# Performance work log

Hardware: AMD Instinct MI355X
Metric: run time of the kernel (lower is better)

The kernel has to match this reference:

```python
import jax, jax.numpy as jnp
import numpy as np

L, H, D, DH, F, V, S, B, CTX = 6, 12, 768, 64, 3072, 32000, 1024, 2, 1024
EPS = 1e-5


def layernorm(x, scale, bias):
    mu = jnp.mean(x, axis=-1, keepdims=True)
    var = jnp.mean(jnp.square(x - mu), axis=-1, keepdims=True)
    return (x - mu) * jax.lax.rsqrt(var + EPS) * scale + bias


def setup_inputs() -> dict:
    key = jax.random.key(0)
    ks = jax.random.split(key, 16)
    std = 0.02
    res_std = 0.02 * (2 * L) ** (-0.5)
    inp = {
        "X": jax.random.randint(ks[0], (B, S), 0, V),
        "emb": jax.random.normal(ks[1], (V, D), jnp.float32) * std,            # tied with head weight
        "pos_emb": jax.random.normal(ks[2], (CTX, D), jnp.float32) * 0.01,
        "Wq": jax.random.normal(ks[3], (L, H, D, DH), jnp.float32) * std,
        "bq": jnp.zeros((L, H, DH), jnp.float32),
        "Wk": jax.random.normal(ks[4], (L, H, D, DH), jnp.float32) * std,
        "bk": jnp.zeros((L, H, DH), jnp.float32),
        "Wv": jax.random.normal(ks[5], (L, H, D, DH), jnp.float32) * std,
        "bv": jnp.zeros((L, H, DH), jnp.float32),
        "Wo": jax.random.normal(ks[6], (L, H * DH, D), jnp.float32) * res_std,  # ResidualScaledLinear
        "bo": jnp.zeros((L, D), jnp.float32),
        "ln1_s": jnp.ones((L, D), jnp.float32),
        "ln1_b": jnp.zeros((L, D), jnp.float32),
        "ln2_s": jnp.ones((L, D), jnp.float32),
        "ln2_b": jnp.zeros((L, D), jnp.float32),
        "W1": jax.random.normal(ks[7], (L, D, F), jnp.float32) * std,
        "b1": jnp.zeros((L, F), jnp.float32),
        "W2": jax.random.normal(ks[8], (L, F, D), jnp.float32) * res_std,       # ResidualScaledLinear
        "b2": jnp.zeros((L, D), jnp.float32),
        "lnf_s": jnp.ones((D,), jnp.float32),
        "lnf_b": jnp.zeros((D,), jnp.float32),
        "head_b": jnp.zeros((V,), jnp.float32),
    }
    return inp


def decoder_forward(X, emb, pos_emb, Wq, bq, Wk, bk, Wv, bv, Wo, bo,
                    ln1_s, ln1_b, ln2_s, ln2_b, W1, b1, W2, b2,
                    lnf_s, lnf_b, head_b):
    seq = X.shape[1]
    x = emb[X] + pos_emb[:seq]                      # [B,S,D]
    causal = jnp.tril(jnp.ones((seq, seq), bool))   # tril mask buffer
    scale = 1.0 / jnp.sqrt(jnp.float32(DH))
    for l in range(L):
        xn = layernorm(x, ln1_s[l], ln1_b[l])
        q = jnp.einsum('bsd,hdk->bhsk', xn, Wq[l]) + bq[l][None, :, None, :]
        k = jnp.einsum('bsd,hdk->bhsk', xn, Wk[l]) + bk[l][None, :, None, :]
        v = jnp.einsum('bsd,hdk->bhsk', xn, Wv[l]) + bv[l][None, :, None, :]
        scores = jnp.einsum('bhsk,bhtk->bhst', q, k) * scale
        scores = jnp.where(causal, scores, -jnp.inf)
        attn = jax.nn.softmax(scores, axis=-1)
        out = jnp.einsum('bhst,bhtk->bshk', attn, v).reshape(x.shape[0], seq, H * DH)
        x = x + out @ Wo[l] + bo[l]
        xn2 = layernorm(x, ln2_s[l], ln2_b[l])
        x = x + jax.nn.relu(xn2 @ W1[l] + b1[l]) @ W2[l] + b2[l]
    x = layernorm(x, lnf_s, lnf_b)
    return x @ emb.T + head_b                       # tied head weight


def reference(X, emb, pos_emb, Wq, bq, Wk, bk, Wv, bv, Wo, bo,
              ln1_s, ln1_b, ln2_s, ln2_b, W1, b1, W2, b2,
              lnf_s, lnf_b, head_b):
    return decoder_forward(X, emb, pos_emb, Wq, bq, Wk, bk, Wv, bv, Wo, bo,
                           ln1_s, ln1_b, ln2_s, ln2_b, W1, b1, W2, b2,
                           lnf_s, lnf_b, head_b)
```

## Files before the change

### kernel.cpp

```cpp
#include <hip/hip_runtime.h>
#include <cstdint>
#include <cstddef>

#define CL 6
#define CH 12
#define CD 768
#define CDH 64
#define CF 3072
#define CV 32000
#define CS 1024
#define CB 2
#define CM (CB*CS)
#define CQS 2304

typedef unsigned short u16;
typedef __bf16 bf16x8 __attribute__((ext_vector_type(8)));
typedef float f32x4 __attribute__((ext_vector_type(4)));

__device__ __forceinline__ float bf2f(u16 u) {
  union { unsigned int i; float f; } c; c.i = ((unsigned int)u) << 16; return c.f;
}
__device__ __forceinline__ u16 f2bf(float f) {
  union { float f; unsigned int i; } c; c.f = f;
  unsigned int lsb = (c.i >> 16) & 1u;
  c.i += 0x7fffu + lsb;
  return (u16)(c.i >> 16);
}

__device__ __forceinline__ void gload16(const u16* g, u16* l) {
  __builtin_amdgcn_global_load_lds(
      (const __attribute__((address_space(1))) void*)g,
      (__attribute__((address_space(3))) void*)l, 16, 0, 0);
}

__global__ __launch_bounds__(256) void convert_kernel(
    const float* __restrict__ src, u16* __restrict__ dst, int total)
{
  int idx = blockIdx.x * 256 + threadIdx.x;
  if (idx < total) dst[idx] = f2bf(src[idx]);
}

__global__ __launch_bounds__(256) void embed_kernel(
    const int* __restrict__ X, const float* __restrict__ emb,
    const float* __restrict__ pos, float* __restrict__ x)
{
  int idx = blockIdx.x * 256 + threadIdx.x;
  int m = idx / CD, d = idx - m * CD;
  int s = m & (CS - 1);
  x[idx] = emb[(size_t)X[m] * CD + d] + pos[s * CD + d];
}

__global__ __launch_bounds__(256) void ln_kernel(
    const float* __restrict__ x, const float* __restrict__ gs,
    const float* __restrict__ gb, u16* __restrict__ out)
{
  __shared__ float rs[4], rss[4];
  int row = blockIdx.x, tid = threadIdx.x;
  const float* xr = x + (size_t)row * CD;
  float a0 = xr[tid], a1 = xr[tid + 256], a2 = xr[tid + 512];
  float s = a0 + a1 + a2;
  float ss = a0 * a0 + a1 * a1 + a2 * a2;
#pragma unroll
  for (int sh = 32; sh > 0; sh >>= 1) {
    s  += __shfl_xor(s, sh, 64);
    ss += __shfl_xor(ss, sh, 64);
  }
  int w = tid >> 6;
  if ((tid & 63) == 0) { rs[w] = s; rss[w] = ss; }
  __syncthreads();
  s  = rs[0] + rs[1] + rs[2] + rs[3];
  ss = rss[0] + rss[1] + rss[2] + rss[3];
  float mu = s * (1.f / CD);
  float inv = rsqrtf(ss * (1.f / CD) - mu * mu + 1e-5f);
  u16* orow = out + (size_t)row * CD;
  orow[tid]       = f2bf((a0 - mu) * inv * gs[tid]       + gb[tid]);
  orow[tid + 256] = f2bf((a1 - mu) * inv * gs[tid + 256] + gb[tid + 256]);
  orow[tid + 512] = f2bf((a2 - mu) * inv * gs[tid + 512] + gb[tid + 512]);
}

__global__ __launch_bounds__(256) void trans_kernel(
    u16* __restrict__ dst, const float* __restrict__ src, int R, int C,
    int PB, long dstL)
{
  __shared__ float st[32][65];
  int r0 = blockIdx.x * 64, c0 = blockIdx.y * 32, bz = blockIdx.z;
  const float* s = src + (size_t)bz * R * C;
  u16* d = dst + (size_t)(bz / PB) * dstL + (size_t)(bz % PB) * R * C;
  int tx = threadIdx.x & 31, ty = threadIdx.x >> 5;
#pragma unroll
  for (int i = 0; i < 8; i++) {
    int r = ty + 8 * i;
    st[tx][r] = s[(size_t)(r0 + r) * C + c0 + tx];
  }
  __syncthreads();
  int j = threadIdx.x & 15, cbase = threadIdx.x >> 4;
#pragma unroll
  for (int i = 0; i < 2; i++) {
    int c = cbase + 16 * i;
    uint2 pk;
    u16* p = (u16*)&pk;
    p[0] = f2bf(st[c][4 * j + 0]);
    p[1] = f2bf(st[c][4 * j + 1]);
    p[2] = f2bf(st[c][4 * j + 2]);
    p[3] = f2bf(st[c][4 * j + 3]);
    *(uint2*)&d[(size_t)(c0 + c) * R + r0 + 4 * j] = pk;
  }
}

__global__ __launch_bounds__(256) void biaspack_kernel(
    const float* __restrict__ bq, const float* __restrict__ bk,
    const float* __restrict__ bv, float* __restrict__ dst)
{
  int idx = blockIdx.x * 256 + threadIdx.x;
  int l = idx / CQS, c = idx - l * CQS;
  float val;
  if (c < 768)       val = bq[l * 768 + c];
  else if (c < 1536) val = bk[l * 768 + c - 768];
  else               val = bv[l * 768 + c - 1536];
  dst[idx] = val;
}

template<bool RES, bool RELU, bool OUTBF>
__global__ __launch_bounds__(256) void gemm64v3_kernel(
    const u16* __restrict__ A, const u16* __restrict__ Bt,
    const float* __restrict__ bias, const float* __restrict__ res,
    void* __restrict__ outp, int M, int N, int K)
{
  __shared__ __align__(16) u16 As[64 * 32];
  __shared__ __align__(16) u16 Bs[64 * 32];
  int tid = threadIdx.x;
  int m0 = blockIdx.y * 64, n0 = blockIdx.x * 64;
  int wv = tid >> 6, ln = tid & 63;
  int quad = ln >> 4, l16 = ln & 15;
  int wm = (wv >> 1) * 32, wn = (wv & 1) * 32;
  int srow = tid >> 2, scol = (tid & 3) * 8;
  const u16* gA = A  + (size_t)(m0 + srow) * K + scol;
  const u16* gB = Bt + (size_t)(n0 + srow) * K + scol;
  u16* lA = As + wv * 512;
  u16* lB = Bs + wv * 512;

  f32x4 acc[2][2];
  acc[0][0] = f32x4{0,0,0,0}; acc[0][1] = f32x4{0,0,0,0};
  acc[1][0] = f32x4{0,0,0,0}; acc[1][1] = f32x4{0,0,0,0};

  for (int kt = 0; kt < K; kt += 32) {
    __syncthreads();
    gload16(gA + kt, lA);
    gload16(gB + kt, lB);
    __syncthreads();
    bf16x8 af[2], bfr[2];
#pragma unroll
    for (int i = 0; i < 2; i++) {
      af[i]  = *reinterpret_cast<const bf16x8*>(&As[(wm + i * 16 + l16) * 32 + quad * 8]);
      bfr[i] = *reinterpret_cast<const bf16x8*>(&Bs[(wn + i * 16 + l16) * 32 + quad * 8]);
    }
#pragma unroll
    for (int i = 0; i < 2; i++)
#pragma unroll
      for (int j = 0; j < 2; j++)
        acc[i][j] = __builtin_amdgcn_mfma_f32_16x16x32_bf16(af[i], bfr[j], acc[i][j], 0, 0, 0);
  }

#pragma unroll
  for (int i = 0; i < 2; i++) {
    int gmb = m0 + wm + i * 16 + quad * 4;
#pragma unroll
    for (int j = 0; j < 2; j++) {
      int gn = n0 + wn + j * 16 + l16;
      float bsv = bias[gn];
#pragma unroll
      for (int rr = 0; rr < 4; rr++) {
        float val = acc[i][j][rr] + bsv;
        if (RELU) val = fmaxf(val, 0.f);
        size_t o = (size_t)(gmb + rr) * N + gn;
        if (RES) val += res[o];
        if (OUTBF) ((u16*)outp)[o] = f2bf(val);
        else       ((float*)outp)[o] = val;
      }
    }
  }
}

template<bool RES, bool RELU, bool OUTBF>
__global__ __launch_bounds__(256) void gemm128_kernel(
    const u16* __restrict__ A, const u16* __restrict__ Bt,
    const float* __restrict__ bias, const float* __restrict__ res,
    void* __restrict__ outp, int M, int N, int K)
{
  __shared__ __align__(16) u16 As[128 * 32];
  __shared__ __align__(16) u16 Bs[128 * 32];
  int tid = threadIdx.x;
  int nbm = M >> 7, nbn = N >> 7, nwg = nbm * nbn;
  int orig = blockIdx.x;
  int q8 = nwg >> 3, r8 = nwg & 7;
  int xcd = orig & 7;
  int t = ((xcd < r8) ? xcd * (q8 + 1) : r8 * (q8 + 1) + (xcd - r8) * q8) + (orig >> 3);
  int bm = t % nbm, bn = t / nbm;
  int m0 = bm << 7, n0 = bn << 7;

  int wv = tid >> 6, ln = tid & 63;
  int quad = ln >> 4, l16 = ln & 15;
  int wr = wv >> 1, wc = wv & 1;

  int srow = wv * 16 + (ln >> 2);
  int scol = (ln & 3) * 8;
  const u16* ga0 = A  + (size_t)(m0 + srow) * K + scol;
  const u16* ga1 = A  + (size_t)(m0 + srow + 64) * K + scol;
  const u16* gb0 = Bt + (size_t)(n0 + srow) * K + scol;
  const u16* gb1 = Bt + (size_t)(n0 + srow + 64) * K + scol;
  u16* lA0 = As + wv * 512;
  u16* lA1 = As + 2048 + wv * 512;
  u16* lB0 = Bs + wv * 512;
  u16* lB1 = Bs + 2048 + wv * 512;

  f32x4 acc[4][4];
#pragma unroll
  for (int i = 0; i < 4; i++)
#pragma unroll
    for (int j = 0; j < 4; j++) acc[i][j] = f32x4{0.f, 0.f, 0.f, 0.f};

  for (int kt = 0; kt < K; kt += 32) {
    __syncthreads();
    gload16(ga0 + kt, lA0);
    gload16(ga1 + kt, lA1);
    gload16(gb0 + kt, lB0);
    gload16(gb1 + kt, lB1);
    __syncthreads();
    bf16x8 af[4], bf[4];
#pragma unroll
    for (int i = 0; i < 4; i++)
      af[i] = *reinterpret_cast<const bf16x8*>(&As[(wr * 64 + i * 16 + l16) * 32 + quad * 8]);
#pragma unroll
    for (int j = 0; j < 4; j++)
      bf[j] = *reinterpret_cast<const bf16x8*>(&Bs[(wc * 64 + j * 16 + l16) * 32 + quad * 8]);
#pragma unroll
    for (int i = 0; i < 4; i++)
#pragma unroll
      for (int j = 0; j < 4; j++)
        acc[i][j] = __builtin_amdgcn_mfma_f32_16x16x32_bf16(af[i], bf[j], acc[i][j], 0, 0, 0);
  }

#pragma unroll
  for (int i = 0; i < 4; i++) {
    int gm = m0 + wr * 64 + i * 16 + quad * 4;
#pragma unroll
    for (int j = 0; j < 4; j++) {
      int gn = n0 + wc * 64 + j * 16 + l16;
      float bsv = bias[gn];
#pragma unroll
      for (int rr = 0; rr < 4; rr++) {
        float val = acc[i][j][rr] + bsv;
        if (RELU) val = fmaxf(val, 0.f);
        size_t oo = (size_t)(gm + rr) * N + gn;
        if (RES) val += res[oo];
        if (OUTBF) ((u16*)outp)[oo] = f2bf(val);
        else       ((float*)outp)[oo] = val;
      }
    }
  }
}

__global__ __launch_bounds__(256) void attn_mfma_kernel(
    const u16* __restrict__ qkv, u16* __restrict__ o)
{
  __shared__ __align__(16) u16 Ks[2][64 * 64];
  __shared__ __align__(16) u16 Vt[2][64 * 64];
  __shared__ __align__(16) u16 Ps[4 * 16 * 64];

  int tid = threadIdx.x;
  int qb = (CS / 64 - 1) - blockIdx.x;
  int h = blockIdx.y, b = blockIdx.z;
  int wid = tid >> 6, lane = tid & 63, quad = lane >> 4, l16 = lane & 15;
  int q0 = qb * 64;
  size_t bh = (size_t)b * CS * CQS + h * CDH;

  const u16* kbase = qkv + bh + 768;
  const u16* vbase = qkv + bh + 1536;

  int t4 = (tid & 15) * 4, dg = (tid >> 4) * 4;

  bf16x8 aq[2];
  {
    const u16* qrow = qkv + bh + (size_t)(q0 + wid * 16 + l16) * CQS;
#pragma unroll
    for (int ks = 0; ks < 2; ks++) {
      uint4 t = *(const uint4*)(qrow + ks * 32 + quad * 8);
      aq[ks] = *reinterpret_cast<bf16x8*>(&t);
    }
  }

  f32x4 oacc[4];
  float mrow[4], lrow[4];
#pragma unroll
  for (int j = 0; j < 4; j++) oacc[j] = f32x4{0.f, 0.f, 0.f, 0.f};
#pragma unroll
  for (int r = 0; r < 4; r++) { mrow[r] = -1e30f; lrow[r] = 0.f; }

  {
#pragma unroll
    for (int it = 0; it < 2; it++) {
      int c = it * 256 + tid;
      int row = c >> 3, c8l = c & 7;
      gload16(kbase + (size_t)row * CQS + (((c8l ^ (row & 7)) * 8)),
              &Ks[0][(it * 256 + wid * 64) * 8]);
    }
    uint2 vr[4];
#pragma unroll
    for (int i = 0; i < 4; i++)
      vr[i] = *(const uint2*)(vbase + (size_t)(t4 + i) * CQS + dg);
#pragma unroll
    for (int j = 0; j < 4; j++) {
      int d = dg + j;
      uint2 pk;
      u16* p = (u16*)&pk;
      p[0] = ((const u16*)&vr[0])[j]; p[1] = ((const u16*)&vr[1])[j];
      p[2] = ((const u16*)&vr[2])[j]; p[3] = ((const u16*)&vr[3])[j];
      *(uint2*)&Vt[0][d * 64 + (((t4 >> 3) ^ (d & 7)) * 8) + (t4 & 4)] = pk;
    }
  }

  for (int t0 = 0; t0 <= q0; t0 += 64) {
    int cur = (t0 >> 6) & 1;
    __syncthreads();
    bool hasnext = (t0 + 64 <= q0);
    uint2 vr[4];
    if (hasnext) {
      const u16* vb2 = vbase + (size_t)(t0 + 64) * CQS;
#pragma unroll
      for (int i = 0; i < 4; i++)
        vr[i] = *(const uint2*)(vb2 + (size_t)(t4 + i) * CQS + dg);
      const u16* kb2 = kbase + (size_t)(t0 + 64) * CQS;
#pragma unroll
      for (int it = 0; it < 2; it++) {
        int c = it * 256 + tid;
        int row = c >> 3, c8l = c & 7;
        gload16(kb2 + (size_t)row * CQS + (((c8l ^ (row & 7)) * 8)),
                &Ks[cur ^ 1][(it * 256 + wid * 64) * 8]);
      }
    }

    f32x4 sacc[4];
#pragma unroll
    for (int j = 0; j < 4; j++) sacc[j] = f32x4{0.f, 0.f, 0.f, 0.f};
#pragma unroll
    for (int j = 0; j < 4; j++) {
      int row = j * 16 + l16;
#pragma unroll
      for (int ks = 0; ks < 2; ks++) {
        bf16x8 bk = *reinterpret_cast<const bf16x8*>(
            &Ks[cur][row * 64 + ((((ks * 4 + quad) ^ (row & 7)) * 8))]);
        sacc[j] = __builtin_amdgcn_mfma_f32_16x16x32_bf16(aq[ks], bk, sacc[j], 0, 0, 0);
      }
    }

    int qg0 = q0 + wid * 16 + quad * 4;
#pragma unroll
    for (int j = 0; j < 4; j++) {
      int tg = t0 + j * 16 + l16;
#pragma unroll
      for (int r = 0; r < 4; r++) {
        float s = sacc[j][r] * 0.125f;
        sacc[j][r] = (tg <= qg0 + r) ? s : -1e30f;
      }
    }

#pragma unroll
    for (int r = 0; r < 4; r++) {
      float m = fmaxf(fmaxf(sacc[0][r], sacc[1][r]), fmaxf(sacc[2][r], sacc[3][r]));
#pragma unroll
      for (int sh = 1; sh < 16; sh <<= 1) m = fmaxf(m, __shfl_xor(m, sh, 64));
      float mnew = fmaxf(mrow[r], m);
      float scal = __expf(mrow[r] - mnew);
      mrow[r] = mnew;
      lrow[r] *= scal;
#pragma unroll
      for (int j = 0; j < 4; j++) oacc[j][r] *= scal;
      float sum = 0.f;
#pragma unroll
      for (int j = 0; j < 4; j++) {
        float p = __expf(sacc[j][r] - mnew);
        sacc[j][r] = p;
        sum += p;
      }
#pragma unroll
      for (int sh = 1; sh < 16; sh <<= 1) sum += __shfl_xor(sum, sh, 64);
      lrow[r] += sum;
    }

    u16* Pw = Ps + wid * 1024;
#pragma unroll
    for (int j = 0; j < 4; j++) {
      int c = (l16 >> 3) + 2 * j;
#pragma unroll
      for (int r = 0; r < 4; r++) {
        int row = quad * 4 + r;
        Pw[row * 64 + (((c ^ (row & 7)) * 8) | (l16 & 7))] = f2bf(sacc[j][r]);
      }
    }

    bf16x8 ap[2];
#pragma unroll
    for (int ks = 0; ks < 2; ks++)
      ap[ks] = *reinterpret_cast<const bf16x8*>(
          &Pw[l16 * 64 + ((((ks * 4 + quad) ^ (l16 & 7)) * 8))]);
#pragma unroll
    for (int j = 0; j < 4; j++) {
      int row = j * 16 + l16;
#pragma unroll
      for (int ks = 0; ks < 2; ks++) {
        bf16x8 bv = *reinterpret_cast<const bf16x8*>(
            &Vt[cur][row * 64 + ((((ks * 4 + quad) ^ (row & 7)) * 8))]);
        oacc[j] = __builtin_amdgcn_mfma_f32_16x16x32_bf16(ap[ks], bv, oacc[j], 0, 0, 0);
      }
    }

    if (hasnext) {
#pragma unroll
      for (int j = 0; j < 4; j++) {
        int d = dg + j;
        uint2 pk;
        u16* p = (u16*)&pk;
        p[0] = ((const u16*)&vr[0])[j]; p[1] = ((const u16*)&vr[1])[j];
        p[2] = ((const u16*)&vr[2])[j]; p[3] = ((const u16*)&vr[3])[j];
        *(uint2*)&Vt[cur ^ 1][d * 64 + (((t4 >> 3) ^ (d & 7)) * 8) + (t4 & 4)] = pk;
      }
    }
  }

#pragma unroll
  for (int r = 0; r < 4; r++) {
    float inv = 1.f / lrow[r];
    int qg = q0 + wid * 16 + quad * 4 + r;
    u16* orow = o + (size_t)b * CS * CD + h * CDH + (size_t)qg * CD;
#pragma unroll
    for (int j = 0; j < 4; j++)
      orow[j * 16 + l16] = f2bf(oacc[j][r] * inv);
  }
}

extern "C" void kernel_launch(void* const* d_in, const int* in_sizes, int n_in,
                              void* d_out, int out_size, void* d_ws, size_t ws_size,
                              hipStream_t stream) {
  const int*   X      = (const int*)d_in[0];
  const float* emb    = (const float*)d_in[1];
  const float* pos    = (const float*)d_in[2];
  const float* Wq     = (const float*)d_in[3];
  const float* bq     = (const float*)d_in[4];
  const float* Wk     = (const float*)d_in[5];
  const float* bk     = (const float*)d_in[6];
  const float* Wv     = (const float*)d_in[7];
  const float* bv     = (const float*)d_in[8];
  const float* Wo     = (const float*)d_in[9];
  const float* bo     = (const float*)d_in[10];
  const float* ln1s   = (const float*)d_in[11];
  const float* ln1b   = (const float*)d_in[12];
  const float* ln2s   = (const float*)d_in[13];
  const float* ln2b   = (const float*)d_in[14];
  const float* W1     = (const float*)d_in[15];
  const float* b1     = (const float*)d_in[16];
  const float* W2     = (const float*)d_in[17];
  const float* b2     = (const float*)d_in[18];
  const float* lnfs   = (const float*)d_in[19];
  const float* lnfb   = (const float*)d_in[20];
  const float* headb  = (const float*)d_in[21];
  (void)in_sizes; (void)n_in; (void)out_size;

  char* ws = (char*)d_ws;
  size_t off = 0;
  auto alloc = [&](size_t bytes) { void* p = ws + off; off += (bytes + 255) & ~(size_t)255; return p; };

  float* x     = (float*)alloc((size_t)CM * CD * 4);
  u16*   xn    = (u16*)  alloc((size_t)CM * CD * 2);
  u16*   qkvb  = (u16*)  alloc((size_t)CM * CQS * 2);
  u16*   ao    = (u16*)  alloc((size_t)CM * CD * 2);
  u16*   hb    = (u16*)  alloc((size_t)CM * CF * 2);
  u16*   embC  = (u16*)  alloc((size_t)CV * CD * 2);
  float* biasp = (float*)alloc((size_t)CL * CQS * 4);

  const size_t WQKV = (size_t)CQS * CD;
  const size_t WOO  = (size_t)CD * CD;
  const size_t WFF  = (size_t)CD * CF;
  size_t perLayerElems = WQKV + WOO + 2 * WFF;
  bool fused = (ws_size >= off + (size_t)CL * perLayerElems * 2 + 4096);
  int LW = fused ? CL : 1;
  u16* Wqkvt = (u16*)alloc((size_t)LW * WQKV * 2);
  u16* Wot   = (u16*)alloc((size_t)LW * WOO * 2);
  u16* W1t   = (u16*)alloc((size_t)LW * WFF * 2);
  u16* W2t   = (u16*)alloc((size_t)LW * WFF * 2);

  embed_kernel<<<CM * CD / 256, 256, 0, stream>>>(X, emb, pos, x);
  convert_kernel<<<(CV * CD) / 256, 256, 0, stream>>>(emb, embC, CV * CD);
  biaspack_kernel<<<(CL * CQS) / 256, 256, 0, stream>>>(bq, bk, bv, biasp);

  if (fused) {
    trans_kernel<<<dim3(CD / 64, CDH / 32, CL * CH), 256, 0, stream>>>(Wqkvt,              Wq, CD, CDH, CH, (long)WQKV);
    trans_kernel<<<dim3(CD / 64, CDH / 32, CL * CH), 256, 0, stream>>>(Wqkvt + 768 * 768,  Wk, CD, CDH, CH, (long)WQKV);
    trans_kernel<<<dim3(CD / 64, CDH / 32, CL * CH), 256, 0, stream>>>(Wqkvt + 1536 * 768, Wv, CD, CDH, CH, (long)WQKV);
    trans_kernel<<<dim3(CD / 64, CD / 32, CL), 256, 0, stream>>>(Wot, Wo, CD, CD, 1, (long)WOO);
    trans_kernel<<<dim3(CD / 64, CF / 32, CL), 256, 0, stream>>>(W1t, W1, CD, CF, 1, (long)WFF);
    trans_kernel<<<dim3(CF / 64, CD / 32, CL), 256, 0, stream>>>(W2t, W2, CF, CD, 1, (long)WFF);
  }

  const int QKV_TOT = CH * CD * CDH;

  for (int l = 0; l < CL; l++) {
    if (!fused) {
      trans_kernel<<<dim3(CD / 64, CDH / 32, CH), 256, 0, stream>>>(Wqkvt,              Wq + (size_t)l * QKV_TOT, CD, CDH, CH, (long)WQKV);
      trans_kernel<<<dim3(CD / 64, CDH / 32, CH), 256, 0, stream>>>(Wqkvt + 768 * 768,  Wk + (size_t)l * QKV_TOT, CD, CDH, CH, (long)WQKV);
      trans_kernel<<<dim3(CD / 64, CDH / 32, CH), 256, 0, stream>>>(Wqkvt + 1536 * 768, Wv + (size_t)l * QKV_TOT, CD, CDH, CH, (long)WQKV);
      trans_kernel<<<dim3(CD / 64, CD / 32, 1), 256, 0, stream>>>(Wot, Wo + (size_t)l * WOO, CD, CD, 1, (long)WOO);
      trans_kernel<<<dim3(CD / 64, CF / 32, 1), 256, 0, stream>>>(W1t, W1 + (size_t)l * WFF, CD, CF, 1, (long)WFF);
      trans_kernel<<<dim3(CF / 64, CD / 32, 1), 256, 0, stream>>>(W2t, W2 + (size_t)l * WFF, CF, CD, 1, (long)WFF);
    }
    int lw = fused ? l : 0;
    const u16* wqkv = Wqkvt + (size_t)lw * WQKV;
    const u16* wot  = Wot   + (size_t)lw * WOO;
    const u16* w1t  = W1t   + (size_t)lw * WFF;
    const u16* w2t  = W2t   + (size_t)lw * WFF;

    ln_kernel<<<CM, 256, 0, stream>>>(x, ln1s + l * CD, ln1b + l * CD, xn);

    gemm128_kernel<false, false, true><<<(CM / 128) * (CQS / 128), 256, 0, stream>>>(
        xn, wqkv, biasp + l * CQS, nullptr, qkvb, CM, CQS, CD);

    attn_mfma_kernel<<<dim3(CS / 64, CH, CB), 256, 0, stream>>>(qkvb, ao);

    gemm64v3_kernel<true, false, false><<<dim3(CD / 64, CM / 64), 256, 0, stream>>>(
        ao, wot, bo + l * CD, x, x, CM, CD, CD);

    ln_kernel<<<CM, 256, 0, stream>>>(x, ln2s + l * CD, ln2b + l * CD, xn);

    gemm128_kernel<false, true, true><<<(CM / 128) * (CF / 128), 256, 0, stream>>>(
        xn, w1t, b1 + l * CF, nullptr, hb, CM, CF, CD);

    gemm64v3_kernel<true, false, false><<<dim3(CD / 64, CM / 64), 256, 0, stream>>>(
        hb, w2t, b2 + l * CD, x, x, CM, CD, CF);
  }

  ln_kernel<<<CM, 256, 0, stream>>>(x, lnfs, lnfb, xn);
  gemm128_kernel<false, false, false><<<(CM / 128) * (CV / 128), 256, 0, stream>>>(
      xn, embC, headb, nullptr, d_out, CM, CV, CD);
}
```

Baseline: 1.570 ms.

## Split long causal attention query blocks across two KV chunks with combine kernel

The eight longest query blocks (qb 8..15) are now each split into two workgroups that process halves of the causal key range. Each half writes unnormalized partial outputs plus row max and sum to a float workspace. A new combine kernel merges the halves with log-sum-exp rescaling. This is meant to cut the tail imbalance of causal attention, where the last blocks do up to 16 tiles, at the cost of an extra launch and workspace traffic.

```diff
diff --git a/kernel.cpp b/kernel.cpp
--- a/kernel.cpp
+++ b/kernel.cpp
@@ -12,6 +12,7 @@
 #define CB 2
 #define CM (CB*CS)
 #define CQS 2304
+#define PSTRIDE 4224
 
 typedef unsigned short u16;
 typedef __bf16 bf16x8 __attribute__((ext_vector_type(8)));
@@ -261,16 +262,25 @@
 }
 
 __global__ __launch_bounds__(256) void attn_mfma_kernel(
-    const u16* __restrict__ qkv, u16* __restrict__ o)
+    const u16* __restrict__ qkv, u16* __restrict__ o, float* __restrict__ part)
 {
   __shared__ __align__(16) u16 Ks[2][64 * 64];
   __shared__ __align__(16) u16 Vt[2][64 * 64];
   __shared__ __align__(16) u16 Ps[4 * 16 * 64];
 
   int tid = threadIdx.x;
-  int qb = (CS / 64 - 1) - blockIdx.x;
+  int a = blockIdx.x;
   int h = blockIdx.y, b = blockIdx.z;
   int wid = tid >> 6, lane = tid & 63, quad = lane >> 4, l16 = lane & 15;
+
+  int qb, ts, te, chunk;
+  if (a < 16) {
+    qb = 15 - (a >> 1);
+    int half = (qb + 1) >> 1;
+    if (a & 1) { ts = 0; te = half - 1; chunk = 0; }
+    else       { ts = half; te = qb;    chunk = 1; }
+  } else { qb = 23 - a; ts = 0; te = qb; chunk = -1; }
+
   int q0 = qb * 64;
   size_t bh = (size_t)b * CS * CQS + h * CDH;
 
@@ -297,17 +307,19 @@
   for (int r = 0; r < 4; r++) { mrow[r] = -1e30f; lrow[r] = 0.f; }
 
   {
+    const u16* kb0 = kbase + (size_t)ts * 64 * CQS;
 #pragma unroll
     for (int it = 0; it < 2; it++) {
       int c = it * 256 + tid;
       int row = c >> 3, c8l = c & 7;
-      gload16(kbase + (size_t)row * CQS + (((c8l ^ (row & 7)) * 8)),
+      gload16(kb0 + (size_t)row * CQS + (((c8l ^ (row & 7)) * 8)),
               &Ks[0][(it * 256 + wid * 64) * 8]);
     }
+    const u16* vb0 = vbase + (size_t)ts * 64 * CQS;
     uint2 vr[4];
 #pragma unroll
     for (int i = 0; i < 4; i++)
-      vr[i] = *(const uint2*)(vbase + (size_t)(t4 + i) * CQS + dg);
+      vr[i] = *(const uint2*)(vb0 + (size_t)(t4 + i) * CQS + dg);
 #pragma unroll
     for (int j = 0; j < 4; j++) {
       int d = dg + j;
@@ -319,10 +331,11 @@
     }
   }
 
-  for (int t0 = 0; t0 <= q0; t0 += 64) {
-    int cur = (t0 >> 6) & 1;
+  for (int tt = ts; tt <= te; tt++) {
+    int t0 = tt * 64;
+    int cur = (tt - ts) & 1;
     __syncthreads();
-    bool hasnext = (t0 + 64 <= q0);
+    bool hasnext = (tt < te);
     uint2 vr[4];
     if (hasnext) {
       const u16* vb2 = vbase + (size_t)(t0 + 64) * CQS;
@@ -427,14 +440,46 @@
     }
   }
 
-#pragma unroll
-  for (int r = 0; r < 4; r++) {
-    float inv = 1.f / lrow[r];
-    int qg = q0 + wid * 16 + quad * 4 + r;
-    u16* orow = o + (size_t)b * CS * CD + h * CDH + (size_t)qg * CD;
-#pragma unroll
-    for (int j = 0; j < 4; j++)
-      orow[j * 16 + l16] = f2bf(oacc[j][r] * inv);
+  if (chunk < 0) {
+#pragma unroll
+    for (int r = 0; r < 4; r++) {
+      float inv = 1.f / lrow[r];
+      int qg = q0 + wid * 16 + quad * 4 + r;
+      u16* orow = o + (size_t)b * CS * CD + h * CDH + (size_t)qg * CD;
+#pragma unroll
+      for (int j = 0; j < 4; j++)
+        orow[j * 16 + l16] = f2bf(oacc[j][r] * inv);
+    }
+  } else {
+    float* Po = part + (size_t)(((b * CH + h) * 8 + (qb - 8)) * 2 + chunk) * PSTRIDE;
+#pragma unroll
+    for (int r = 0; r < 4; r++) {
+      int row = wid * 16 + quad * 4 + r;
+#pragma unroll
+      for (int j = 0; j < 4; j++)
+        Po[row * 64 + j * 16 + l16] = oacc[j][r];
+      if (l16 == 0) { Po[4096 + row] = mrow[r]; Po[4160 + row] = lrow[r]; }
+    }
+  }
+}
+
+__global__ __launch_bounds__(256) void attn_combine_kernel(
+    const float* __restrict__ part, u16* __restrict__ o)
+{
+  int qb = 8 + blockIdx.x, h = blockIdx.y, b = blockIdx.z;
+  const float* P0 = part + (size_t)(((b * CH + h) * 8 + (qb - 8)) * 2) * PSTRIDE;
+  const float* P1 = P0 + PSTRIDE;
+  int t = threadIdx.x;
+  int row = t >> 2, c0 = (t & 3) * 16;
+  float m0 = P0[4096 + row], m1 = P1[4096 + row];
+  float m = fmaxf(m0, m1);
+  float w0 = __expf(m0 - m), w1 = __expf(m1 - m);
+  float inv = 1.f / (P0[4160 + row] * w0 + P1[4160 + row] * w1);
+  u16* orow = o + (size_t)b * CS * CD + h * CDH + (size_t)(qb * 64 + row) * CD;
+#pragma unroll
+  for (int j = 0; j < 16; j++) {
+    int col = c0 + j;
+    orow[col] = f2bf((P0[row * 64 + col] * w0 + P1[row * 64 + col] * w1) * inv);
   }
 }
 
@@ -476,6 +521,7 @@
   u16*   hb    = (u16*)  alloc((size_t)CM * CF * 2);
   u16*   embC  = (u16*)  alloc((size_t)CV * CD * 2);
   float* biasp = (float*)alloc((size_t)CL * CQS * 4);
+  float* part  = (float*)alloc((size_t)CB * CH * 8 * 2 * PSTRIDE * 4);
 
   const size_t WQKV = (size_t)CQS * CD;
   const size_t WOO  = (size_t)CD * CD;
@@ -523,7 +569,8 @@
     gemm128_kernel<false, false, true><<<(CM / 128) * (CQS / 128), 256, 0, stream>>>(
         xn, wqkv, biasp + l * CQS, nullptr, qkvb, CM, CQS, CD);
 
-    attn_mfma_kernel<<<dim3(CS / 64, CH, CB), 256, 0, stream>>>(qkvb, ao);
+    attn_mfma_kernel<<<dim3(24, CH, CB), 256, 0, stream>>>(qkvb, ao, part);
+    attn_combine_kernel<<<dim3(8, CH, CB), 256, 0, stream>>>(part, ao);
 
     gemm64v3_kernel<true, false, false><<<dim3(CD / 64, CM / 64), 256, 0, stream>>>(
         ao, wot, bo + l * CD, x, x, CM, CD, CD);
```

Result: faster. 1.508 ms (-4.0%).
